# Kernel tuning notes

Hardware: AMD Instinct MI355X
Metric: run time of the kernel (lower is better)

Reference implementation:

```python
import jax, jax.numpy as jnp
import numpy as np

HEADS = 8
OUT_PER_HEAD = 9
NEG_SLOPE = 0.2  # PyG GATConv default


def setup_inputs() -> dict:
    key = jax.random.key(0)
    k1, k2, k3, k4, k5, k6 = jax.random.split(key, 6)
    N, F_in, E = 100000, 12, 1600000
    x = jax.random.normal(k1, (N, F_in), dtype=jnp.float32)
    edge_index = jax.random.randint(k2, (2, E), 0, N, dtype=jnp.int64)
    # GATConv params: lin weight [F_in, H*C], attention vectors a_src/a_dst [H, C], bias [C] (concat=False)
    s = 1.0 / np.sqrt(F_in)
    W = jax.random.uniform(k3, (F_in, HEADS * OUT_PER_HEAD), minval=-s, maxval=s, dtype=jnp.float32)
    a_src = jax.random.uniform(k4, (HEADS, OUT_PER_HEAD), minval=-s, maxval=s, dtype=jnp.float32)
    a_dst = jax.random.uniform(k5, (HEADS, OUT_PER_HEAD), minval=-s, maxval=s, dtype=jnp.float32)
    bias = jnp.zeros((OUT_PER_HEAD,), dtype=jnp.float32)
    return {"x": x, "edge_index": edge_index, "W": W, "a_src": a_src, "a_dst": a_dst, "bias": bias}


def reference(x, edge_index, W, a_src, a_dst, bias):
    N = x.shape[0]
    # add self-loops (PyG GATConv default add_self_loops=True)
    loops = jnp.arange(N, dtype=edge_index.dtype)
    src = jnp.concatenate([edge_index[0], loops])
    dst = jnp.concatenate([edge_index[1], loops])
    # per-head linear transform: [N, H, C]
    h = (x @ W).reshape(N, HEADS, OUT_PER_HEAD)
    # node-level attention halves: [N, H]
    al_src = jnp.einsum('nhc,hc->nh', h, a_src)
    al_dst = jnp.einsum('nhc,hc->nh', h, a_dst)
    # edge-wise logits [E, H]
    e = jax.nn.leaky_relu(al_src[src] + al_dst[dst], NEG_SLOPE)
    # segment softmax over incoming edges of each destination node
    m = jax.ops.segment_max(e, dst, num_segments=N)  # [N, H]
    ex = jnp.exp(e - m[dst])
    denom = jax.ops.segment_sum(ex, dst, num_segments=N)  # [N, H]
    alpha = ex / (denom[dst] + jnp.float32(1e-16))
    # weighted scatter-aggregate: [N, H, C]
    out = jax.ops.segment_sum(alpha[:, :, None] * h[src], dst, num_segments=N)
    # concat=False -> mean over heads, then bias
    out = out.mean(axis=1) + bias
    # dropout is identity in eval; final log_softmax over feature dim
    return jax.nn.log_softmax(out, axis=1)
```

## Files before the change

kernel.cpp:

```cpp
#include <hip/hip_runtime.h>
#include <math.h>

#define NHEADS 8
#define NC 9
#define NHC 72
#define FIN 12
#define WAVES_PER_BLOCK 4
#define ROWW 48
#define ALS_OFF 36
#define MAXBUK 512
#define TILE 4096

__device__ __forceinline__ float lrelu(float v) { return v > 0.f ? v : 0.2f * v; }

__device__ __forceinline__ unsigned pack_bf16(float a, float b) {
    unsigned ua = __float_as_uint(a); ua += 0x7fffu + ((ua >> 16) & 1u);
    unsigned ub = __float_as_uint(b); ub += 0x7fffu + ((ub >> 16) & 1u);
    return (ua >> 16) | (ub & 0xffff0000u);
}

__global__ void __launch_bounds__(256) k_transform(
    const float* __restrict__ x, const float* __restrict__ W,
    const float* __restrict__ a_src, const float* __restrict__ a_dst,
    unsigned* __restrict__ hrow, float* __restrict__ al_d,
    const int* __restrict__ dst, int* __restrict__ bucket_count,
    int N, int E, int nbuk)
{
    __shared__ float sW[FIN * NHC];
    __shared__ float sas[NHC];
    __shared__ float sad[NHC];
    __shared__ int bcnt[MAXBUK];
    int tid = threadIdx.x;
    for (int i = tid; i < FIN * NHC; i += blockDim.x) sW[i] = W[i];
    if (tid < NHC) { sas[tid] = a_src[tid]; sad[tid] = a_dst[tid]; }
    for (int i = tid; i < nbuk; i += blockDim.x) bcnt[i] = 0;
    __syncthreads();
    int n = blockIdx.x * blockDim.x + tid;
    if (n < N) {
        float xv[FIN];
        const float4* xp = reinterpret_cast<const float4*>(x + (size_t)n * FIN);
        float4 q0 = xp[0], q1 = xp[1], q2 = xp[2];
        xv[0] = q0.x; xv[1] = q0.y; xv[2] = q0.z; xv[3] = q0.w;
        xv[4] = q1.x; xv[5] = q1.y; xv[6] = q1.z; xv[7] = q1.w;
        xv[8] = q2.x; xv[9] = q2.y; xv[10] = q2.z; xv[11] = q2.w;

        float acc[NHC];
        #pragma unroll
        for (int j = 0; j < NHC; ++j) acc[j] = 0.f;
        #pragma unroll
        for (int k = 0; k < FIN; ++k) {
            float xk = xv[k];
            #pragma unroll
            for (int j = 0; j < NHC; ++j) acc[j] = fmaf(xk, sW[k * NHC + j], acc[j]);
        }

        unsigned* rp = hrow + (size_t)n * ROWW;
        #pragma unroll
        for (int l = 0; l < NHC / 2; ++l)
            rp[l] = pack_bf16(acc[2 * l], acc[2 * l + 1]);

        float* rf = reinterpret_cast<float*>(rp);
        #pragma unroll
        for (int hh = 0; hh < NHEADS; ++hh) {
            float ss = 0.f, dd = 0.f;
            #pragma unroll
            for (int c = 0; c < NC; ++c) {
                ss = fmaf(acc[hh * NC + c], sas[hh * NC + c], ss);
                dd = fmaf(acc[hh * NC + c], sad[hh * NC + c], dd);
            }
            rf[ALS_OFF + hh] = ss;
            al_d[(size_t)n * NHEADS + hh] = dd;
        }
    }
    int stride = gridDim.x * blockDim.x;
    for (int i = blockIdx.x * blockDim.x + tid; i < E; i += stride)
        atomicAdd(&bcnt[dst[i] >> 8], 1);
    __syncthreads();
    for (int i = tid; i < nbuk; i += blockDim.x)
        if (bcnt[i]) atomicAdd(&bucket_count[i], bcnt[i]);
}

__global__ void __launch_bounds__(512) k_bscan(
    const int* __restrict__ bucket_count, int* __restrict__ bucket_base,
    int* __restrict__ gcur, int* __restrict__ rowptr, int nbuk, int N, int E)
{
    __shared__ int s[512];
    int t = threadIdx.x;
    int v = (t < nbuk) ? bucket_count[t] : 0;
    s[t] = v;
    __syncthreads();
    for (int off = 1; off < 512; off <<= 1) {
        int u = (t >= off) ? s[t - off] : 0;
        __syncthreads();
        s[t] += u;
        __syncthreads();
    }
    if (t < nbuk) {
        int ex = s[t] - v;
        bucket_base[t] = ex;
        gcur[t] = ex;
    }
    if (t == 0) { bucket_base[nbuk] = E; rowptr[N] = E; }
}

__global__ void __launch_bounds__(256) k_bucketA(
    const int* __restrict__ src, const int* __restrict__ dst,
    int* __restrict__ gcur, unsigned* __restrict__ bpair, int E, int nbuk)
{
    __shared__ int cnt[MAXBUK];
    __shared__ int sbase[MAXBUK];
    int t = threadIdx.x;
    for (int i = t; i < nbuk; i += 256) cnt[i] = 0;
    __syncthreads();
    int base0 = blockIdx.x * TILE;
    int rk[16], bk[16];
    unsigned pk[16];
    #pragma unroll
    for (int j = 0; j < 16; ++j) {
        int i = base0 + j * 256 + t;
        if (i < E) {
            int d = dst[i];
            int sg = src[i];
            bk[j] = d >> 8;
            pk[j] = (unsigned)sg | ((unsigned)(d & 255) << 24);
            rk[j] = atomicAdd(&cnt[bk[j]], 1);
        } else bk[j] = -1;
    }
    __syncthreads();
    for (int b = t; b < nbuk; b += 256)
        if (cnt[b]) sbase[b] = atomicAdd(&gcur[b], cnt[b]);
    __syncthreads();
    #pragma unroll
    for (int j = 0; j < 16; ++j)
        if (bk[j] >= 0) bpair[sbase[bk[j]] + rk[j]] = pk[j];
}

__global__ void __launch_bounds__(256) k_bucketB(
    const unsigned* __restrict__ bpair, const int* __restrict__ bucket_base,
    int* __restrict__ rowptr, int* __restrict__ sorted_off, int N)
{
    __shared__ int cnt[256];
    __shared__ int sc[256];
    int b = blockIdx.x;
    int t = threadIdx.x;
    int lo = bucket_base[b], hi = bucket_base[b + 1];
    cnt[t] = 0;
    __syncthreads();
    for (int i = lo + t; i < hi; i += 256)
        atomicAdd(&cnt[bpair[i] >> 24], 1);
    __syncthreads();
    int v = cnt[t];
    sc[t] = v;
    __syncthreads();
    for (int off = 1; off < 256; off <<= 1) {
        int u = (t >= off) ? sc[t - off] : 0;
        __syncthreads();
        sc[t] += u;
        __syncthreads();
    }
    int excl = sc[t] - v;
    int node = (b << 8) + t;
    if (node < N) rowptr[node] = lo + excl;
    __syncthreads();
    cnt[t] = lo + excl;
    __syncthreads();
    for (int i = lo + t; i < hi; i += 256) {
        unsigned w = bpair[i];
        int pos = atomicAdd(&cnt[w >> 24], 1);
        sorted_off[pos] = (int)((w & 0xFFFFFFu) * (ROWW * 4u));
    }
}

__global__ void __launch_bounds__(256) k_gat(
    const int* __restrict__ rowptr, const int* __restrict__ sorted_off,
    const unsigned* __restrict__ hrow, const float* __restrict__ al_d,
    const float* __restrict__ bias, float* __restrict__ out, int N)
{
    __shared__ int   s_off[WAVES_PER_BLOCK][64];
    __shared__ float s_ex[WAVES_PER_BLOCK][64][9];
    __shared__ float s_den[WAVES_PER_BLOCK][8];
    __shared__ float s_out[WAVES_PER_BLOCK][NHC];
    __shared__ float s_v[WAVES_PER_BLOCK][NC];

    int wid  = threadIdx.x >> 6;
    int lane = threadIdx.x & 63;
    int n = blockIdx.x * WAVES_PER_BLOCK + wid;
    if (n >= N) return;

    int base  = rowptr[n];
    int total = rowptr[n + 1] - base + 1;

    int g  = lane >> 3;
    int hh = lane & 7;
    float ald_h = al_d[(size_t)n * NHEADS + hh];

    bool act36 = lane < NHC / 2;
    int widx4 = act36 ? lane * 4 : 0;
    int c0 = 2 * lane, c1 = 2 * lane + 1;
    int ha = act36 ? c0 / NC : 0;
    int hb = act36 ? c1 / NC : 0;
    float accA = 0.f, accB = 0.f;
    float den_part = 0.f;

    const char* hbase = reinterpret_cast<const char*>(hrow);
    int als_boff = (ALS_OFF + hh) * 4;
    int self_off = n * (ROWW * 4);

    for (int cb = 0; cb < total; cb += 64) {
        int rem = total - cb;
        int clen = rem < 64 ? rem : 64;
        int clenR = (clen + 3) & ~3;

        int j = cb + lane;
        int off_l = self_off;
        if (j < total - 1) off_l = sorted_off[base + j];
        s_off[wid][lane] = off_l;

        for (int k = 0; k * 8 < clenR; ++k) {
            int lj = k * 8 + g;
            int off = s_off[wid][lj];
            float als = *reinterpret_cast<const float*>(hbase + off + als_boff);
            float ex = 0.f;
            if (cb + lj < total) ex = __expf(lrelu(als + ald_h));
            s_ex[wid][lj][hh] = ex;
            den_part += ex;
        }

        for (int e = 0; e < clenR; e += 4) {
            #pragma unroll
            for (int p = 0; p < 4; ++p) {
                int ee = e + p;
                int off = s_off[wid][ee];
                unsigned w = *reinterpret_cast<const unsigned*>(hbase + off + widx4);
                float fa = __uint_as_float(w << 16);
                float fb = __uint_as_float(w & 0xffff0000u);
                accA = fmaf(s_ex[wid][ee][ha], fa, accA);
                accB = fmaf(s_ex[wid][ee][hb], fb, accB);
            }
        }
    }

    den_part += __shfl_xor(den_part, 8, 64);
    den_part += __shfl_xor(den_part, 16, 64);
    den_part += __shfl_xor(den_part, 32, 64);
    if (lane < 8) s_den[wid][lane] = den_part;

    if (act36) {
        float ia = 1.f / (s_den[wid][ha] + 1e-16f);
        float ib = 1.f / (s_den[wid][hb] + 1e-16f);
        s_out[wid][c0] = accA * ia;
        s_out[wid][c1] = accB * ib;
    }

    if (lane < NC) {
        float v = 0.f;
        #pragma unroll
        for (int h = 0; h < NHEADS; ++h) v += s_out[wid][h * NC + lane];
        v = v * (1.f / NHEADS) + bias[lane];
        s_v[wid][lane] = v;
        float mx = -INFINITY;
        #pragma unroll
        for (int c = 0; c < NC; ++c) mx = fmaxf(mx, s_v[wid][c]);
        float sum = 0.f;
        #pragma unroll
        for (int c = 0; c < NC; ++c) sum += __expf(s_v[wid][c] - mx);
        float lse = mx + __logf(sum);
        out[(size_t)n * NC + lane] = s_v[wid][lane] - lse;
    }
}

extern "C" void kernel_launch(void* const* d_in, const int* in_sizes, int n_in,
                              void* d_out, int out_size, void* d_ws, size_t ws_size,
                              hipStream_t stream)
{
    const float* x     = (const float*)d_in[0];
    const int*   ei    = (const int*)d_in[1];
    const float* W     = (const float*)d_in[2];
    const float* a_src = (const float*)d_in[3];
    const float* a_dst = (const float*)d_in[4];
    const float* bias  = (const float*)d_in[5];

    int N = in_sizes[0] / FIN;
    int E = in_sizes[1] / 2;
    const int* src = ei;
    const int* dst = ei + E;
    int nbuk = (N + 255) >> 8;

    char* ws = (char*)d_ws;
    unsigned* hrow = (unsigned*)ws;     ws += (size_t)N * ROWW * sizeof(unsigned);
    float* al_d = (float*)ws;           ws += (size_t)N * NHEADS * sizeof(float);
    int* rowptr = (int*)ws;             ws += (size_t)(N + 1) * sizeof(int);
    int* bucket_count = (int*)ws;       ws += (size_t)(MAXBUK + 1) * sizeof(int);
    int* bucket_base  = (int*)ws;       ws += (size_t)(MAXBUK + 1) * sizeof(int);
    int* gcur = (int*)ws;               ws += (size_t)MAXBUK * sizeof(int);
    unsigned* bpair = (unsigned*)ws;    ws += (size_t)E * sizeof(unsigned);
    int* sorted_off = (int*)ws;         ws += (size_t)E * sizeof(int);

    hipMemsetAsync(bucket_count, 0, (size_t)(MAXBUK + 1) * sizeof(int), stream);

    int nb_n = (N + 255) / 256;
    int nb_a = (E + TILE - 1) / TILE;

    k_transform<<<nb_n, 256, 0, stream>>>(x, W, a_src, a_dst, hrow, al_d,
                                          dst, bucket_count, N, E, nbuk);
    k_bscan<<<1, 512, 0, stream>>>(bucket_count, bucket_base, gcur, rowptr,
                                   nbuk, N, E);
    k_bucketA<<<nb_a, 256, 0, stream>>>(src, dst, gcur, bpair, E, nbuk);
    k_bucketB<<<nbuk, 256, 0, stream>>>(bpair, bucket_base, rowptr, sorted_off, N);

    int nb_g = (N + WAVES_PER_BLOCK - 1) / WAVES_PER_BLOCK;
    k_gat<<<nb_g, 256, 0, stream>>>(rowptr, sorted_off, hrow, al_d, bias,
                                    (float*)d_out, N);
}
```

Before: 168.9 us.

## Pad per-head bf16 rows so each lane's pair stays within one head; readlane offsets

Changes the packed node row layout so each head occupies 5 bf16 pairs (the 9th channel padded with zero), which moves the attention-source scalars to offset 40. In the aggregation loop each lane now reads one shared exp weight for both of its channels instead of two LDS lookups for potentially different heads. The per-edge offset is taken from the lane register via readlane instead of shared memory. It uses 40 lanes instead of 36 and four more row words, but the row stride is unchanged.

```diff
diff --git a/kernel.cpp b/kernel.cpp
--- a/kernel.cpp
+++ b/kernel.cpp
@@ -7,7 +7,7 @@
 #define FIN 12
 #define WAVES_PER_BLOCK 4
 #define ROWW 48
-#define ALS_OFF 36
+#define ALS_OFF 40
 #define MAXBUK 512
 #define TILE 4096
 
@@ -18,6 +18,8 @@
     unsigned ub = __float_as_uint(b); ub += 0x7fffu + ((ub >> 16) & 1u);
     return (ua >> 16) | (ub & 0xffff0000u);
 }
+__device__ __forceinline__ float blo(unsigned w) { return __uint_as_float(w << 16); }
+__device__ __forceinline__ float bhi(unsigned w) { return __uint_as_float(w & 0xffff0000u); }
 
 __global__ void __launch_bounds__(256) k_transform(
     const float* __restrict__ x, const float* __restrict__ W,
@@ -56,8 +58,14 @@
 
         unsigned* rp = hrow + (size_t)n * ROWW;
         #pragma unroll
-        for (int l = 0; l < NHC / 2; ++l)
-            rp[l] = pack_bf16(acc[2 * l], acc[2 * l + 1]);
+        for (int hh = 0; hh < NHEADS; ++hh) {
+            const float* A = acc + hh * NC;
+            rp[5 * hh + 0] = pack_bf16(A[0], A[1]);
+            rp[5 * hh + 1] = pack_bf16(A[2], A[3]);
+            rp[5 * hh + 2] = pack_bf16(A[4], A[5]);
+            rp[5 * hh + 3] = pack_bf16(A[6], A[7]);
+            rp[5 * hh + 4] = pack_bf16(A[8], 0.f);
+        }
 
         float* rf = reinterpret_cast<float*>(rp);
         #pragma unroll
@@ -194,11 +202,11 @@
     int hh = lane & 7;
     float ald_h = al_d[(size_t)n * NHEADS + hh];
 
-    bool act36 = lane < NHC / 2;
-    int widx4 = act36 ? lane * 4 : 0;
-    int c0 = 2 * lane, c1 = 2 * lane + 1;
-    int ha = act36 ? c0 / NC : 0;
-    int hb = act36 ? c1 / NC : 0;
+    bool act40 = lane < 40;
+    int h_agg = act40 ? lane / 5 : 0;
+    int i_agg = act40 ? lane - h_agg * 5 : 4;
+    int widx4 = act40 ? lane * 4 : 0;
+    int c0 = h_agg * NC + 2 * i_agg;
     float accA = 0.f, accB = 0.f;
     float den_part = 0.f;
 
@@ -230,12 +238,11 @@
             #pragma unroll
             for (int p = 0; p < 4; ++p) {
                 int ee = e + p;
-                int off = s_off[wid][ee];
+                int off = __builtin_amdgcn_readlane(off_l, ee);
                 unsigned w = *reinterpret_cast<const unsigned*>(hbase + off + widx4);
-                float fa = __uint_as_float(w << 16);
-                float fb = __uint_as_float(w & 0xffff0000u);
-                accA = fmaf(s_ex[wid][ee][ha], fa, accA);
-                accB = fmaf(s_ex[wid][ee][hb], fb, accB);
+                float ex1 = s_ex[wid][ee][h_agg];
+                accA = fmaf(ex1, blo(w), accA);
+                accB = fmaf(ex1, bhi(w), accB);
             }
         }
     }
@@ -245,11 +252,10 @@
     den_part += __shfl_xor(den_part, 32, 64);
     if (lane < 8) s_den[wid][lane] = den_part;
 
-    if (act36) {
-        float ia = 1.f / (s_den[wid][ha] + 1e-16f);
-        float ib = 1.f / (s_den[wid][hb] + 1e-16f);
-        s_out[wid][c0] = accA * ia;
-        s_out[wid][c1] = accB * ib;
+    if (act40) {
+        float inv = 1.f / (s_den[wid][h_agg] + 1e-16f);
+        s_out[wid][c0] = accA * inv;
+        if (i_agg < 4) s_out[wid][c0 + 1] = accB * inv;
     }
 
     if (lane < NC) {
```

New measurement: 172.2 us. About the same (+2.0%).
